# Optimization experiments

Measured on AMD Instinct MI355X. Metric: run time of the kernel, lower is better.

Reference implementation:

```python
import jax, jax.numpy as jnp
import numpy as np

T, B, IN, H, L = 512, 32, 512, 512, 2  # seq_len, batch, input_size, hidden_size, num_layers
D = 2  # bidirectional
EPS = 1e-5


def setup_inputs() -> dict:
    key = jax.random.key(0)
    ks = jax.random.split(key, 4)
    s = 0.05
    return {
        "x": jax.random.normal(ks[0], (T, B, IN), jnp.float32),
        "h0": jnp.zeros((L * D, B, H), jnp.float32),
        # stacked per (layer, direction) params; index = 2*layer + dir (dir 0 = fwd, 1 = back)
        "Wx": jax.random.normal(ks[1], (L * D, IN, 3 * H), jnp.float32) * s,
        "Wh": jax.random.normal(ks[2], (L * D, H, 3 * H), jnp.float32) * s,
        "bx": jnp.zeros((L * D, 3 * H), jnp.float32),
        "bh": jnp.zeros((L * D, 3 * H), jnp.float32),
        "gx": jnp.ones((L * D, 3 * H), jnp.float32),   # LN affine scale for input proj
        "bex": jnp.zeros((L * D, 3 * H), jnp.float32), # LN affine shift for input proj
        "gh": jnp.ones((L * D, 3 * H), jnp.float32),   # LN affine scale for recurrent proj
        "beh": jnp.zeros((L * D, 3 * H), jnp.float32), # LN affine shift for recurrent proj
    }


def _ln3(a, g, b):
    # per-gate LayerNorm: a is [B, 3H]; normalize each H-sized gate chunk
    Bn, H3 = a.shape
    Hh = H3 // 3
    a = a.reshape(Bn, 3, Hh)
    mu = a.mean(-1, keepdims=True)
    var = ((a - mu) ** 2).mean(-1, keepdims=True)
    a = (a - mu) * jax.lax.rsqrt(var + EPS)
    a = a * g.reshape(3, Hh) + b.reshape(3, Hh)
    return a.reshape(Bn, H3)


def _run_dir(xs, h, Wx, Wh, bx, bh, gx, bex, gh, beh):
    # xs: [T, B, F], h: [B, H]; scan LNGRU cell over time
    def step(h, x):
        ax = _ln3(x @ Wx + bx, gx, bex)
        ah = _ln3(h @ Wh + bh, gh, beh)
        axr, axz, axn = jnp.split(ax, 3, axis=-1)
        ahr, ahz, ahn = jnp.split(ah, 3, axis=-1)
        r = jax.nn.sigmoid(axr + ahr)
        z = jax.nn.sigmoid(axz + ahz)
        n = jnp.tanh(axn + r * ahn)
        h_new = (1.0 - z) * n + z * h
        return h_new, h_new
    hT, ys = jax.lax.scan(step, h, xs)
    return hT, ys


def reference(x, h0, Wx, Wh, bx, bh, gx, bex, gh, beh):
    ff, back = x, x
    hiddens = []
    for layer in range(L):
        i = 2 * layer
        hT, ff = _run_dir(ff, h0[i], Wx[i], Wh[i], bx[i], bh[i], gx[i], bex[i], gh[i], beh[i])
        hiddens.append(hT)
        j = 2 * layer + 1
        hT, yb = _run_dir(back[::-1], h0[j], Wx[j], Wh[j], bx[j], bh[j], gx[j], bex[j], gh[j], beh[j])
        back = yb[::-1]
        hiddens.append(hT)
    output = jnp.concatenate([ff, back], axis=-1)  # [T, B, 2H]
    return output, jnp.stack(hiddens)  # hiddens: [L*2, B, H]
```

## Files before the change

kernel.cpp:

```cpp
#include <hip/hip_runtime.h>

#define T_N 512
#define B_N 32
#define H_N 512
#define G3 1536
#define NBLK 192
#define NGRP 8
#define GRPSZ (NBLK / NGRP)
#define NT 1024
#define EPS_LN 1e-5f
#define OUT_HID_OFF (T_N * B_N * 1024)

#define WS_STATS 320
#define WS_DOTS  (WS_STATS + 1536)
#define WS_HBUF  (WS_DOTS + 4 * B_N * G3)
#define WS_Y0    (WS_HBUF + 2 * B_N * H_N)

#define WLDS_F 32256
#define HL_F   8256
#define LDS_BYTES ((WLDS_F + HL_F + 256) * 4)

__device__ __forceinline__ float cload(const float* p) {
  return __hip_atomic_load(p, __ATOMIC_RELAXED, __HIP_MEMORY_SCOPE_AGENT);
}
__device__ __forceinline__ void cstore(float* p, float v) {
  __hip_atomic_store(p, v, __ATOMIC_RELAXED, __HIP_MEMORY_SCOPE_AGENT);
}
union U64F2 { unsigned long long u; float f[2]; };
__device__ __forceinline__ U64F2 cload2(const float* p) {
  U64F2 r;
  r.u = __hip_atomic_load((const unsigned long long*)p, __ATOMIC_RELAXED,
                          __HIP_MEMORY_SCOPE_AGENT);
  return r;
}

__device__ __forceinline__ void gbar(unsigned* barbase, unsigned& epoch, int grp) {
  epoch++;
  __builtin_amdgcn_s_waitcnt(0);
  __syncthreads();
  if (threadIdx.x == 0) {
    unsigned* gc  = barbase + grp * 32;
    unsigned* top = barbase + NGRP * 32;
    unsigned* rel = barbase + NGRP * 32 + 32;
    unsigned r = __hip_atomic_fetch_add(gc, 1u, __ATOMIC_RELAXED, __HIP_MEMORY_SCOPE_AGENT);
    if (r == epoch * GRPSZ - 1u) {
      unsigned r2 = __hip_atomic_fetch_add(top, 1u, __ATOMIC_RELAXED, __HIP_MEMORY_SCOPE_AGENT);
      if (r2 == epoch * NGRP - 1u)
        __hip_atomic_store(rel, epoch, __ATOMIC_RELAXED, __HIP_MEMORY_SCOPE_AGENT);
    }
    while (__hip_atomic_load(rel, __ATOMIC_RELAXED, __HIP_MEMORY_SCOPE_AGENT) < epoch)
      __builtin_amdgcn_s_sleep(1);
  }
  __syncthreads();
}

#define FMA16(WA, WB, R1, R2) do { \
  acc[0][0][0]=fmaf((R1).x,(WA).x,acc[0][0][0]); acc[0][0][1]=fmaf((R1).y,(WA).y,acc[0][0][1]); \
  acc[0][0][2]=fmaf((R1).z,(WA).z,acc[0][0][2]); acc[0][0][3]=fmaf((R1).w,(WA).w,acc[0][0][3]); \
  acc[0][1][0]=fmaf((R2).x,(WA).x,acc[0][1][0]); acc[0][1][1]=fmaf((R2).y,(WA).y,acc[0][1][1]); \
  acc[0][1][2]=fmaf((R2).z,(WA).z,acc[0][1][2]); acc[0][1][3]=fmaf((R2).w,(WA).w,acc[0][1][3]); \
  acc[1][0][0]=fmaf((R1).x,(WB).x,acc[1][0][0]); acc[1][0][1]=fmaf((R1).y,(WB).y,acc[1][0][1]); \
  acc[1][0][2]=fmaf((R1).z,(WB).z,acc[1][0][2]); acc[1][0][3]=fmaf((R1).w,(WB).w,acc[1][0][3]); \
  acc[1][1][0]=fmaf((R2).x,(WB).x,acc[1][1][0]); acc[1][1][1]=fmaf((R2).y,(WB).y,acc[1][1][1]); \
  acc[1][1][2]=fmaf((R2).z,(WB).z,acc[1][1][2]); acc[1][1][3]=fmaf((R2).w,(WB).w,acc[1][1][3]); \
} while (0)

__global__ void __launch_bounds__(NT, 1)
lngru9(const float* __restrict__ x, const float* __restrict__ h0,
       const float* __restrict__ Wx, const float* __restrict__ Wh,
       const float* __restrict__ bx, const float* __restrict__ bh,
       const float* __restrict__ gx, const float* __restrict__ bex,
       const float* __restrict__ gh, const float* __restrict__ beh,
       float* __restrict__ out, float* __restrict__ ws)
{
  extern __shared__ __align__(16) float smem[];
  float* wlds = smem;
  float* hl   = smem + WLDS_F;
  float* sred = smem + WLDS_F + HL_F;

  unsigned* barbase = (unsigned*)ws;
  float* stats = ws + WS_STATS;
  float* dots  = ws + WS_DOTS;
  float* hbuf  = ws + WS_HBUF;
  float* y0    = ws + WS_Y0;

  const int tid  = threadIdx.x;
  const int lane = tid & 63;
  const int wv   = tid >> 6;
  const int bid  = blockIdx.x;
  const int grp  = bid & 7;
  const int bs   = bid & 1;
  const int jt   = (bid >> 1) % 24;
  const int kd   = (bid >> 1) / 24;
  const int kind = kd & 1;
  const int d    = kd >> 1;
  const int j0   = jt * 64;
  const int g    = jt >> 3;
  const int b0   = bs * 16;
  const bool is_gate = (kind == 0) && (jt < 8);

  const bool gw  = (wv < 4);
  const int jq   = wv & 3;
  const int jj   = lane & 7;
  const int boct = lane >> 3;
  const int jla  = jq * 8 + jj;
  const int jlb  = jla + 32;

  unsigned epoch = 0;

  for (int ph = 0; ph < 2; ++ph) {
    const int widx = ph * 2 + d;

    const float* wgl = (kind ? Wh : Wx) + (size_t)widx * H_N * G3 + j0;
    for (int kk = 0; kk < 32; ++kk) {
      int k = wv * 32 + kk;
      if (k < 504)
        wlds[(k >> 2) * 256 + lane * 4 + (k & 3)] = wgl[(size_t)k * G3 + lane];
    }
    float4 wt[2][2];
    if (gw) {
#pragma unroll
      for (int h = 0; h < 2; ++h) {
        wt[0][h].x = wgl[(size_t)(504 + 4*h + 0) * G3 + jla];
        wt[0][h].y = wgl[(size_t)(504 + 4*h + 1) * G3 + jla];
        wt[0][h].z = wgl[(size_t)(504 + 4*h + 2) * G3 + jla];
        wt[0][h].w = wgl[(size_t)(504 + 4*h + 3) * G3 + jla];
        wt[1][h].x = wgl[(size_t)(504 + 4*h + 0) * G3 + jlb];
        wt[1][h].y = wgl[(size_t)(504 + 4*h + 1) * G3 + jlb];
        wt[1][h].z = wgl[(size_t)(504 + 4*h + 2) * G3 + jlb];
        wt[1][h].w = wgl[(size_t)(504 + 4*h + 3) * G3 + jlb];
      }
    }

    if (is_gate) {
      cstore(&hbuf[(d * B_N + b0 + wv) * H_N + j0 + lane],
             h0[(widx * B_N + b0 + wv) * H_N + j0 + lane]);
    }
    gbar(barbase, epoch, grp);

    const float  bva  = (kind ? bh : bx)[widx * G3 + j0 + jla];
    const float  bvb  = (kind ? bh : bx)[widx * G3 + j0 + jlb];
    const float* xsrc = (ph == 0) ? x : (y0 + (size_t)d * T_N * B_N * H_N);
    const float* hsrc = hbuf + (d * B_N + b0) * H_N;
    const float4* wqa = (const float4*)wlds + jla;
    const float4* wqb = (const float4*)wlds + jlb;
    const float*  h1  = hl + boct * 516;
    const float*  h2  = hl + (boct + 8) * 516;

    for (int s = 0; s < T_N; ++s) {
      const int t = d ? (T_N - 1 - s) : s;
      const int p = s & 1;
      float* stp = stats + p * 768;

      if (kind) {
#pragma unroll
        for (int q = 0; q < 4; ++q) {
          int e = (tid + q * 1024) * 2;
          U64F2 v = cload2(hsrc + e);
          int bb = e >> 9, k = e & 511;
          hl[bb * 516 + k]     = v.f[0];
          hl[bb * 516 + k + 1] = v.f[1];
        }
        __syncthreads();
      }

      float acc[2][2][4] = {{{0.f,0.f,0.f,0.f},{0.f,0.f,0.f,0.f}},
                            {{0.f,0.f,0.f,0.f},{0.f,0.f,0.f,0.f}}};
      if (gw) {
        if (kind) {
#pragma unroll 3
          for (int k4 = 0; k4 < 126; ++k4) {
            float4 wa = wqa[k4 * 64];
            float4 wb = wqb[k4 * 64];
            float4 r1 = *(const float4*)(h1 + k4 * 4);
            float4 r2 = *(const float4*)(h2 + k4 * 4);
            FMA16(wa, wb, r1, r2);
          }
          {
            float4 r1a = *(const float4*)(h1 + 504);
            float4 r1b = *(const float4*)(h1 + 508);
            float4 r2a = *(const float4*)(h2 + 504);
            float4 r2b = *(const float4*)(h2 + 508);
            FMA16(wt[0][0], wt[1][0], r1a, r2a);
            FMA16(wt[0][1], wt[1][1], r1b, r2b);
          }
        } else {
          const float* rp1 = xsrc + ((size_t)t * B_N + b0 + boct) * H_N;
          const float* rp2 = rp1 + 8 * H_N;
#pragma unroll 6
          for (int k4 = 0; k4 < 126; ++k4) {
            float4 wa = wqa[k4 * 64];
            float4 wb = wqb[k4 * 64];
            float4 r1 = *(const float4*)(rp1 + k4 * 4);
            float4 r2 = *(const float4*)(rp2 + k4 * 4);
            FMA16(wa, wb, r1, r2);
          }
          {
            float4 r1a = *(const float4*)(rp1 + 504);
            float4 r1b = *(const float4*)(rp1 + 508);
            float4 r2a = *(const float4*)(rp2 + 504);
            float4 r2b = *(const float4*)(rp2 + 508);
            FMA16(wt[0][0], wt[1][0], r1a, r2a);
            FMA16(wt[0][1], wt[1][1], r1b, r2b);
          }
        }
      }

      if (gw) {
        float ta1 = bva + (acc[0][0][0] + acc[0][0][1]) + (acc[0][0][2] + acc[0][0][3]);
        float ta2 = bva + (acc[0][1][0] + acc[0][1][1]) + (acc[0][1][2] + acc[0][1][3]);
        float tb1 = bvb + (acc[1][0][0] + acc[1][0][1]) + (acc[1][0][2] + acc[1][0][3]);
        float tb2 = bvb + (acc[1][1][0] + acc[1][1][1]) + (acc[1][1][2] + acc[1][1][3]);

        float* dr1 = &dots[(size_t)(kd * B_N + b0 + boct) * G3 + j0];
        float* dr2 = dr1 + (size_t)8 * G3;
        cstore(dr1 + jla, ta1);
        cstore(dr1 + jlb, tb1);
        cstore(dr2 + jla, ta2);
        cstore(dr2 + jlb, tb2);

        float s1a = ta1 + tb1, s2a = ta1 * ta1 + tb1 * tb1;
        float s1b = ta2 + tb2, s2b = ta2 * ta2 + tb2 * tb2;
        s1a += __shfl_xor(s1a, 1, 64); s2a += __shfl_xor(s2a, 1, 64);
        s1b += __shfl_xor(s1b, 1, 64); s2b += __shfl_xor(s2b, 1, 64);
        s1a += __shfl_xor(s1a, 2, 64); s2a += __shfl_xor(s2a, 2, 64);
        s1b += __shfl_xor(s1b, 2, 64); s2b += __shfl_xor(s2b, 2, 64);
        s1a += __shfl_xor(s1a, 4, 64); s2a += __shfl_xor(s2a, 4, 64);
        s1b += __shfl_xor(s1b, 4, 64); s2b += __shfl_xor(s2b, 4, 64);
        if (jj == 0) {
          sred[(boct * 4 + jq) * 2 + 0] = s1a;
          sred[(boct * 4 + jq) * 2 + 1] = s2a;
          sred[((boct + 8) * 4 + jq) * 2 + 0] = s1b;
          sred[((boct + 8) * 4 + jq) * 2 + 1] = s2b;
        }
      }
      __syncthreads();
      if (tid < 32) {
        int bl = tid >> 1, st = tid & 1;
        float a2 = 0.f;
#pragma unroll
        for (int q = 0; q < 4; ++q) a2 += sred[(bl * 4 + q) * 2 + st];
        atomicAdd(&stp[((kd * 3 + g) * B_N + b0 + bl) * 2 + st], a2);
      }

      gbar(barbase, epoch, grp);

      if (bid == NBLK - 1) {
        float* so = stats + (p ^ 1) * 768;
        if (tid < 768) cstore(so + tid, 0.f);
      }
      if (is_gate) {
        const int c  = j0 + lane;
        const int gb = b0 + wv;
        float a[2][3];
#pragma unroll
        for (int k2 = 0; k2 < 2; ++k2) {
          const float* dr  = dots + ((d * 2 + k2) * B_N + gb) * G3;
          const float* gam = (k2 ? gh : gx) + widx * G3;
          const float* bet = (k2 ? beh : bex) + widx * G3;
#pragma unroll
          for (int g2 = 0; g2 < 3; ++g2) {
            float v = cload(dr + g2 * H_N + c);
            const float* sl = stp + (((d * 2 + k2) * 3 + g2) * B_N + gb) * 2;
            float mu  = cload(sl)     * (1.f / 512.f);
            float var = cload(sl + 1) * (1.f / 512.f) - mu * mu;
            float inv = rsqrtf(var + EPS_LN);
            int J = g2 * H_N + c;
            a[k2][g2] = (v - mu) * inv * gam[J] + bet[J];
          }
        }
        float r = 1.f / (1.f + __expf(-(a[0][0] + a[1][0])));
        float z = 1.f / (1.f + __expf(-(a[0][1] + a[1][1])));
        float n = tanhf(a[0][2] + r * a[1][2]);
        float* hp = hbuf + (d * B_N + gb) * H_N + c;
        float hnew = (1.f - z) * n + z * cload(hp);
        cstore(hp, hnew);
        if (ph == 0) {
          cstore(&y0[(((size_t)d * T_N + t) * B_N + gb) * H_N + c], hnew);
        } else {
          out[((size_t)t * B_N + gb) * 1024 + d * H_N + c] = hnew;
        }
        if (s == T_N - 1) {
          out[OUT_HID_OFF + (widx * B_N + gb) * H_N + c] = hnew;
        }
      }
      gbar(barbase, epoch, grp);
    }
  }
}

extern "C" void kernel_launch(void* const* d_in, const int* in_sizes, int n_in,
                              void* d_out, int out_size, void* d_ws, size_t ws_size,
                              hipStream_t stream) {
  const float* x    = (const float*)d_in[0];
  const float* h0   = (const float*)d_in[1];
  const float* Wx   = (const float*)d_in[2];
  const float* Wh   = (const float*)d_in[3];
  const float* bxp  = (const float*)d_in[4];
  const float* bhp  = (const float*)d_in[5];
  const float* gxp  = (const float*)d_in[6];
  const float* bexp = (const float*)d_in[7];
  const float* ghp  = (const float*)d_in[8];
  const float* behp = (const float*)d_in[9];
  float* out = (float*)d_out;
  float* ws  = (float*)d_ws;

  hipMemsetAsync(d_ws, 0, 8192, stream);

  hipFuncSetAttribute((const void*)lngru9,
                      hipFuncAttributeMaxDynamicSharedMemorySize, LDS_BYTES);

  void* args[] = {(void*)&x, (void*)&h0, (void*)&Wx, (void*)&Wh, (void*)&bxp, (void*)&bhp,
                  (void*)&gxp, (void*)&bexp, (void*)&ghp, (void*)&behp, (void*)&out, (void*)&ws};
  hipLaunchCooperativeKernel((void*)lngru9, dim3(NBLK), dim3(NT), args, LDS_BYTES, stream);
}
```

Measured before the change: 22.21 ms.

## Halve grid barriers per step by redundant gate update and pipelined input projection

Every recurrent-projection block now keeps its own copy of the batch's hidden state in LDS and recomputes the full gate update for 512 columns itself. This removes the global hbuf round-trip and one of the two grid barriers per timestep. The input projection is computed one step ahead into a triple-buffered slot, and the stats buffers are widened to four slots so zeroing can happen without an extra barrier. Each wave now handles four 8-column groups with two compute waves instead of four. The cost is redundant elementwise gate work in every kind=1 block, fewer active compute waves per block, and more workspace.

After: 27.09 ms. +22.0%, slower.

```diff
diff --git a/kernel.cpp b/kernel.cpp
--- a/kernel.cpp
+++ b/kernel.cpp
@@ -12,9 +12,11 @@
 #define OUT_HID_OFF (T_N * B_N * 1024)
 
 #define WS_STATS 320
-#define WS_DOTS  (WS_STATS + 1536)
-#define WS_HBUF  (WS_DOTS + 4 * B_N * G3)
-#define WS_Y0    (WS_HBUF + 2 * B_N * H_N)
+#define STSLOT   768
+#define WS_AXD   (WS_STATS + 4 * STSLOT)
+#define DSLOT    (2 * B_N * G3)
+#define WS_AHD   (WS_AXD + 3 * DSLOT)
+#define WS_Y0    (WS_AHD + 2 * DSLOT)
 
 #define WLDS_F 32256
 #define HL_F   8256
@@ -25,13 +27,6 @@
 }
 __device__ __forceinline__ void cstore(float* p, float v) {
   __hip_atomic_store(p, v, __ATOMIC_RELAXED, __HIP_MEMORY_SCOPE_AGENT);
-}
-union U64F2 { unsigned long long u; float f[2]; };
-__device__ __forceinline__ U64F2 cload2(const float* p) {
-  U64F2 r;
-  r.u = __hip_atomic_load((const unsigned long long*)p, __ATOMIC_RELAXED,
-                          __HIP_MEMORY_SCOPE_AGENT);
-  return r;
 }
 
 __device__ __forceinline__ void gbar(unsigned* barbase, unsigned& epoch, int grp) {
@@ -54,24 +49,20 @@
   __syncthreads();
 }
 
-#define FMA16(WA, WB, R1, R2) do { \
-  acc[0][0][0]=fmaf((R1).x,(WA).x,acc[0][0][0]); acc[0][0][1]=fmaf((R1).y,(WA).y,acc[0][0][1]); \
-  acc[0][0][2]=fmaf((R1).z,(WA).z,acc[0][0][2]); acc[0][0][3]=fmaf((R1).w,(WA).w,acc[0][0][3]); \
-  acc[0][1][0]=fmaf((R2).x,(WA).x,acc[0][1][0]); acc[0][1][1]=fmaf((R2).y,(WA).y,acc[0][1][1]); \
-  acc[0][1][2]=fmaf((R2).z,(WA).z,acc[0][1][2]); acc[0][1][3]=fmaf((R2).w,(WA).w,acc[0][1][3]); \
-  acc[1][0][0]=fmaf((R1).x,(WB).x,acc[1][0][0]); acc[1][0][1]=fmaf((R1).y,(WB).y,acc[1][0][1]); \
-  acc[1][0][2]=fmaf((R1).z,(WB).z,acc[1][0][2]); acc[1][0][3]=fmaf((R1).w,(WB).w,acc[1][0][3]); \
-  acc[1][1][0]=fmaf((R2).x,(WB).x,acc[1][1][0]); acc[1][1][1]=fmaf((R2).y,(WB).y,acc[1][1][1]); \
-  acc[1][1][2]=fmaf((R2).z,(WB).z,acc[1][1][2]); acc[1][1][3]=fmaf((R2).w,(WB).w,acc[1][1][3]); \
+#define FMA_M(M, W, R1, R2) do { \
+  acc[M][0][0]=fmaf((R1).x,(W).x,acc[M][0][0]); acc[M][0][1]=fmaf((R1).y,(W).y,acc[M][0][1]); \
+  acc[M][0][2]=fmaf((R1).z,(W).z,acc[M][0][2]); acc[M][0][3]=fmaf((R1).w,(W).w,acc[M][0][3]); \
+  acc[M][1][0]=fmaf((R2).x,(W).x,acc[M][1][0]); acc[M][1][1]=fmaf((R2).y,(W).y,acc[M][1][1]); \
+  acc[M][1][2]=fmaf((R2).z,(W).z,acc[M][1][2]); acc[M][1][3]=fmaf((R2).w,(W).w,acc[M][1][3]); \
 } while (0)
 
 __global__ void __launch_bounds__(NT, 1)
-lngru9(const float* __restrict__ x, const float* __restrict__ h0,
-       const float* __restrict__ Wx, const float* __restrict__ Wh,
-       const float* __restrict__ bx, const float* __restrict__ bh,
-       const float* __restrict__ gx, const float* __restrict__ bex,
-       const float* __restrict__ gh, const float* __restrict__ beh,
-       float* __restrict__ out, float* __restrict__ ws)
+lngru10(const float* __restrict__ x, const float* __restrict__ h0,
+        const float* __restrict__ Wx, const float* __restrict__ Wh,
+        const float* __restrict__ bx, const float* __restrict__ bh,
+        const float* __restrict__ gx, const float* __restrict__ bex,
+        const float* __restrict__ gh, const float* __restrict__ beh,
+        float* __restrict__ out, float* __restrict__ ws)
 {
   extern __shared__ __align__(16) float smem[];
   float* wlds = smem;
@@ -80,8 +71,8 @@
 
   unsigned* barbase = (unsigned*)ws;
   float* stats = ws + WS_STATS;
-  float* dots  = ws + WS_DOTS;
-  float* hbuf  = ws + WS_HBUF;
+  float* axd   = ws + WS_AXD;
+  float* ahd   = ws + WS_AHD;
   float* y0    = ws + WS_Y0;
 
   const int tid  = threadIdx.x;
@@ -97,19 +88,19 @@
   const int j0   = jt * 64;
   const int g    = jt >> 3;
   const int b0   = bs * 16;
-  const bool is_gate = (kind == 0) && (jt < 8);
-
-  const bool gw  = (wv < 4);
-  const int jq   = wv & 3;
+  const bool writer = (kind == 1) && (jt == 0);
+
+  const bool gw  = (wv < 2);
+  const int jq   = wv & 1;
   const int jj   = lane & 7;
   const int boct = lane >> 3;
-  const int jla  = jq * 8 + jj;
-  const int jlb  = jla + 32;
 
   unsigned epoch = 0;
 
   for (int ph = 0; ph < 2; ++ph) {
     const int widx = ph * 2 + d;
+
+    gbar(barbase, epoch, grp);
 
     const float* wgl = (kind ? Wh : Wx) + (size_t)widx * H_N * G3 + j0;
     for (int kk = 0; kk < 32; ++kk) {
@@ -117,110 +108,98 @@
       if (k < 504)
         wlds[(k >> 2) * 256 + lane * 4 + (k & 3)] = wgl[(size_t)k * G3 + lane];
     }
-    float4 wt[2][2];
+    float4 wt[4][2];
+    float  bva[4];
     if (gw) {
 #pragma unroll
-      for (int h = 0; h < 2; ++h) {
-        wt[0][h].x = wgl[(size_t)(504 + 4*h + 0) * G3 + jla];
-        wt[0][h].y = wgl[(size_t)(504 + 4*h + 1) * G3 + jla];
-        wt[0][h].z = wgl[(size_t)(504 + 4*h + 2) * G3 + jla];
-        wt[0][h].w = wgl[(size_t)(504 + 4*h + 3) * G3 + jla];
-        wt[1][h].x = wgl[(size_t)(504 + 4*h + 0) * G3 + jlb];
-        wt[1][h].y = wgl[(size_t)(504 + 4*h + 1) * G3 + jlb];
-        wt[1][h].z = wgl[(size_t)(504 + 4*h + 2) * G3 + jlb];
-        wt[1][h].w = wgl[(size_t)(504 + 4*h + 3) * G3 + jlb];
-      }
-    }
-
-    if (is_gate) {
-      cstore(&hbuf[(d * B_N + b0 + wv) * H_N + j0 + lane],
-             h0[(widx * B_N + b0 + wv) * H_N + j0 + lane]);
-    }
-    gbar(barbase, epoch, grp);
-
-    const float  bva  = (kind ? bh : bx)[widx * G3 + j0 + jla];
-    const float  bvb  = (kind ? bh : bx)[widx * G3 + j0 + jlb];
+      for (int m = 0; m < 4; ++m) {
+        const int jl = jq * 32 + m * 8 + jj;
+        bva[m] = (kind ? bh : bx)[widx * G3 + j0 + jl];
+#pragma unroll
+        for (int h = 0; h < 2; ++h) {
+          wt[m][h].x = wgl[(size_t)(504 + 4*h + 0) * G3 + jl];
+          wt[m][h].y = wgl[(size_t)(504 + 4*h + 1) * G3 + jl];
+          wt[m][h].z = wgl[(size_t)(504 + 4*h + 2) * G3 + jl];
+          wt[m][h].w = wgl[(size_t)(504 + 4*h + 3) * G3 + jl];
+        }
+      }
+    }
+    if (kind) {
+#pragma unroll
+      for (int q = 0; q < 8; ++q)
+        hl[wv * 516 + lane + 64*q] =
+            h0[((size_t)widx * B_N + b0 + wv) * H_N + lane + 64*q];
+    }
+    __syncthreads();
+
     const float* xsrc = (ph == 0) ? x : (y0 + (size_t)d * T_N * B_N * H_N);
-    const float* hsrc = hbuf + (d * B_N + b0) * H_N;
-    const float4* wqa = (const float4*)wlds + jla;
-    const float4* wqb = (const float4*)wlds + jlb;
-    const float*  h1  = hl + boct * 516;
-    const float*  h2  = hl + (boct + 8) * 516;
-
-    for (int s = 0; s < T_N; ++s) {
-      const int t = d ? (T_N - 1 - s) : s;
-      const int p = s & 1;
-      float* stp = stats + p * 768;
-
-      if (kind) {
-#pragma unroll
-        for (int q = 0; q < 4; ++q) {
-          int e = (tid + q * 1024) * 2;
-          U64F2 v = cload2(hsrc + e);
-          int bb = e >> 9, k = e & 511;
-          hl[bb * 516 + k]     = v.f[0];
-          hl[bb * 516 + k + 1] = v.f[1];
-        }
-        __syncthreads();
-      }
-
-      float acc[2][2][4] = {{{0.f,0.f,0.f,0.f},{0.f,0.f,0.f,0.f}},
-                            {{0.f,0.f,0.f,0.f},{0.f,0.f,0.f,0.f}}};
+    const float4* wbase = (const float4*)wlds + jq * 32 + jj;
+
+    auto run_step = [&](int ss) {
+      float acc[4][2][4] = {};
       if (gw) {
         if (kind) {
+          const float* h1 = hl + boct * 516;
+          const float* h2 = h1 + 8 * 516;
 #pragma unroll 3
           for (int k4 = 0; k4 < 126; ++k4) {
-            float4 wa = wqa[k4 * 64];
-            float4 wb = wqb[k4 * 64];
-            float4 r1 = *(const float4*)(h1 + k4 * 4);
-            float4 r2 = *(const float4*)(h2 + k4 * 4);
-            FMA16(wa, wb, r1, r2);
+            float4 w0 = wbase[k4*64 + 0];
+            float4 w1 = wbase[k4*64 + 8];
+            float4 w2 = wbase[k4*64 + 16];
+            float4 w3 = wbase[k4*64 + 24];
+            float4 r1 = *(const float4*)(h1 + k4*4);
+            float4 r2 = *(const float4*)(h2 + k4*4);
+            FMA_M(0,w0,r1,r2); FMA_M(1,w1,r1,r2);
+            FMA_M(2,w2,r1,r2); FMA_M(3,w3,r1,r2);
           }
-          {
-            float4 r1a = *(const float4*)(h1 + 504);
-            float4 r1b = *(const float4*)(h1 + 508);
-            float4 r2a = *(const float4*)(h2 + 504);
-            float4 r2b = *(const float4*)(h2 + 508);
-            FMA16(wt[0][0], wt[1][0], r1a, r2a);
-            FMA16(wt[0][1], wt[1][1], r1b, r2b);
-          }
+          float4 r1a = *(const float4*)(h1 + 504);
+          float4 r1b = *(const float4*)(h1 + 508);
+          float4 r2a = *(const float4*)(h2 + 504);
+          float4 r2b = *(const float4*)(h2 + 508);
+          FMA_M(0,wt[0][0],r1a,r2a); FMA_M(1,wt[1][0],r1a,r2a);
+          FMA_M(2,wt[2][0],r1a,r2a); FMA_M(3,wt[3][0],r1a,r2a);
+          FMA_M(0,wt[0][1],r1b,r2b); FMA_M(1,wt[1][1],r1b,r2b);
+          FMA_M(2,wt[2][1],r1b,r2b); FMA_M(3,wt[3][1],r1b,r2b);
         } else {
+          const int t = d ? (T_N - 1 - ss) : ss;
           const float* rp1 = xsrc + ((size_t)t * B_N + b0 + boct) * H_N;
           const float* rp2 = rp1 + 8 * H_N;
-#pragma unroll 6
+#pragma unroll 4
           for (int k4 = 0; k4 < 126; ++k4) {
-            float4 wa = wqa[k4 * 64];
-            float4 wb = wqb[k4 * 64];
-            float4 r1 = *(const float4*)(rp1 + k4 * 4);
-            float4 r2 = *(const float4*)(rp2 + k4 * 4);
-            FMA16(wa, wb, r1, r2);
+            float4 w0 = wbase[k4*64 + 0];
+            float4 w1 = wbase[k4*64 + 8];
+            float4 w2 = wbase[k4*64 + 16];
+            float4 w3 = wbase[k4*64 + 24];
+            float4 r1 = *(const float4*)(rp1 + k4*4);
+            float4 r2 = *(const float4*)(rp2 + k4*4);
+            FMA_M(0,w0,r1,r2); FMA_M(1,w1,r1,r2);
+            FMA_M(2,w2,r1,r2); FMA_M(3,w3,r1,r2);
           }
-          {
-            float4 r1a = *(const float4*)(rp1 + 504);
-            float4 r1b = *(const float4*)(rp1 + 508);
-            float4 r2a = *(const float4*)(rp2 + 504);
-            float4 r2b = *(const float4*)(rp2 + 508);
-            FMA16(wt[0][0], wt[1][0], r1a, r2a);
-            FMA16(wt[0][1], wt[1][1], r1b, r2b);
-          }
-        }
-      }
-
+          float4 r1a = *(const float4*)(rp1 + 504);
+          float4 r1b = *(const float4*)(rp1 + 508);
+          float4 r2a = *(const float4*)(rp2 + 504);
+          float4 r2b = *(const float4*)(rp2 + 508);
+          FMA_M(0,wt[0][0],r1a,r2a); FMA_M(1,wt[1][0],r1a,r2a);
+          FMA_M(2,wt[2][0],r1a,r2a); FMA_M(3,wt[3][0],r1a,r2a);
+          FMA_M(0,wt[0][1],r1b,r2b); FMA_M(1,wt[1][1],r1b,r2b);
+          FMA_M(2,wt[2][1],r1b,r2b); FMA_M(3,wt[3][1],r1b,r2b);
+        }
+      }
+      float* dd  = kind ? (ahd + (ss & 1) * DSLOT) : (axd + (ss % 3) * DSLOT);
+      float* stp = stats + (ss & 3) * STSLOT;
       if (gw) {
-        float ta1 = bva + (acc[0][0][0] + acc[0][0][1]) + (acc[0][0][2] + acc[0][0][3]);
-        float ta2 = bva + (acc[0][1][0] + acc[0][1][1]) + (acc[0][1][2] + acc[0][1][3]);
-        float tb1 = bvb + (acc[1][0][0] + acc[1][0][1]) + (acc[1][0][2] + acc[1][0][3]);
-        float tb2 = bvb + (acc[1][1][0] + acc[1][1][1]) + (acc[1][1][2] + acc[1][1][3]);
-
-        float* dr1 = &dots[(size_t)(kd * B_N + b0 + boct) * G3 + j0];
+        float* dr1 = dd + (size_t)(d * B_N + b0 + boct) * G3 + j0;
         float* dr2 = dr1 + (size_t)8 * G3;
-        cstore(dr1 + jla, ta1);
-        cstore(dr1 + jlb, tb1);
-        cstore(dr2 + jla, ta2);
-        cstore(dr2 + jlb, tb2);
-
-        float s1a = ta1 + tb1, s2a = ta1 * ta1 + tb1 * tb1;
-        float s1b = ta2 + tb2, s2b = ta2 * ta2 + tb2 * tb2;
+        float s1a = 0.f, s2a = 0.f, s1b = 0.f, s2b = 0.f;
+#pragma unroll
+        for (int m = 0; m < 4; ++m) {
+          const int jl = jq * 32 + m * 8 + jj;
+          float t1 = bva[m] + ((acc[m][0][0]+acc[m][0][1]) + (acc[m][0][2]+acc[m][0][3]));
+          float t2 = bva[m] + ((acc[m][1][0]+acc[m][1][1]) + (acc[m][1][2]+acc[m][1][3]));
+          cstore(dr1 + jl, t1);
+          cstore(dr2 + jl, t2);
+          s1a += t1; s2a += t1 * t1; s1b += t2; s2b += t2 * t2;
+        }
         s1a += __shfl_xor(s1a, 1, 64); s2a += __shfl_xor(s2a, 1, 64);
         s1b += __shfl_xor(s1b, 1, 64); s2b += __shfl_xor(s2b, 1, 64);
         s1a += __shfl_xor(s1a, 2, 64); s2a += __shfl_xor(s2a, 2, 64);
@@ -228,63 +207,87 @@
         s1a += __shfl_xor(s1a, 4, 64); s2a += __shfl_xor(s2a, 4, 64);
         s1b += __shfl_xor(s1b, 4, 64); s2b += __shfl_xor(s2b, 4, 64);
         if (jj == 0) {
-          sred[(boct * 4 + jq) * 2 + 0] = s1a;
-          sred[(boct * 4 + jq) * 2 + 1] = s2a;
-          sred[((boct + 8) * 4 + jq) * 2 + 0] = s1b;
-          sred[((boct + 8) * 4 + jq) * 2 + 1] = s2b;
+          sred[boct * 4 + jq * 2 + 0] = s1a;
+          sred[boct * 4 + jq * 2 + 1] = s2a;
+          sred[(boct + 8) * 4 + jq * 2 + 0] = s1b;
+          sred[(boct + 8) * 4 + jq * 2 + 1] = s2b;
         }
       }
       __syncthreads();
       if (tid < 32) {
         int bl = tid >> 1, st = tid & 1;
-        float a2 = 0.f;
-#pragma unroll
-        for (int q = 0; q < 4; ++q) a2 += sred[(bl * 4 + q) * 2 + st];
+        float a2 = sred[bl * 4 + st] + sred[bl * 4 + 2 + st];
         atomicAdd(&stp[((kd * 3 + g) * B_N + b0 + bl) * 2 + st], a2);
       }
+    };
+
+    if (!kind) run_step(0);
+    gbar(barbase, epoch, grp);
+
+    for (int s = 0; s < T_N; ++s) {
+      if (kind) run_step(s);
+      else if (s < T_N - 1) run_step(s + 1);
+
+      if (bid == NBLK - 1) {
+        float* so = stats + ((s + 2) & 3) * STSLOT;
+        if (tid < 768) cstore(so + tid, 0.f);
+      }
 
       gbar(barbase, epoch, grp);
 
-      if (bid == NBLK - 1) {
-        float* so = stats + (p ^ 1) * 768;
-        if (tid < 768) cstore(so + tid, 0.f);
-      }
-      if (is_gate) {
-        const int c  = j0 + lane;
+      if (kind) {
+        const int t  = d ? (T_N - 1 - s) : s;
         const int gb = b0 + wv;
-        float a[2][3];
-#pragma unroll
-        for (int k2 = 0; k2 < 2; ++k2) {
-          const float* dr  = dots + ((d * 2 + k2) * B_N + gb) * G3;
-          const float* gam = (k2 ? gh : gx) + widx * G3;
-          const float* bet = (k2 ? beh : bex) + widx * G3;
+        const float* axr = axd + (s % 3) * DSLOT + (size_t)(d * B_N + gb) * G3;
+        const float* ahr = ahd + (s & 1) * DSLOT + (size_t)(d * B_N + gb) * G3;
+        const float* stp = stats + (s & 3) * STSLOT;
+        float mu[2][3], inv[2][3];
+#pragma unroll
+        for (int k2 = 0; k2 < 2; ++k2)
 #pragma unroll
           for (int g2 = 0; g2 < 3; ++g2) {
-            float v = cload(dr + g2 * H_N + c);
             const float* sl = stp + (((d * 2 + k2) * 3 + g2) * B_N + gb) * 2;
-            float mu  = cload(sl)     * (1.f / 512.f);
-            float var = cload(sl + 1) * (1.f / 512.f) - mu * mu;
-            float inv = rsqrtf(var + EPS_LN);
-            int J = g2 * H_N + c;
-            a[k2][g2] = (v - mu) * inv * gam[J] + bet[J];
+            float m1 = cload(sl)     * (1.f / 512.f);
+            float m2 = cload(sl + 1) * (1.f / 512.f);
+            mu[k2][g2]  = m1;
+            inv[k2][g2] = rsqrtf(m2 - m1 * m1 + EPS_LN);
           }
-        }
-        float r = 1.f / (1.f + __expf(-(a[0][0] + a[1][0])));
-        float z = 1.f / (1.f + __expf(-(a[0][1] + a[1][1])));
-        float n = tanhf(a[0][2] + r * a[1][2]);
-        float* hp = hbuf + (d * B_N + gb) * H_N + c;
-        float hnew = (1.f - z) * n + z * cload(hp);
-        cstore(hp, hnew);
-        if (ph == 0) {
-          cstore(&y0[(((size_t)d * T_N + t) * B_N + gb) * H_N + c], hnew);
-        } else {
-          out[((size_t)t * B_N + gb) * 1024 + d * H_N + c] = hnew;
-        }
-        if (s == T_N - 1) {
-          out[OUT_HID_OFF + (widx * B_N + gb) * H_N + c] = hnew;
-        }
-      }
-      gbar(barbase, epoch, grp);
+        const float* gxr = gx  + widx * G3;
+        const float* bxr = bex + widx * G3;
+        const float* ghr = gh  + widx * G3;
+        const float* bhr = beh + widx * G3;
+#pragma unroll 2
+        for (int q = 0; q < 8; ++q) {
+          const int c = lane + 64 * q;
+          float ax0 = cload(axr + c);
+          float ax1 = cload(axr + H_N + c);
+          float ax2 = cload(axr + 2 * H_N + c);
+          float ah0 = cload(ahr + c);
+          float ah1 = cload(ahr + H_N + c);
+          float ah2 = cload(ahr + 2 * H_N + c);
+          float a00 = (ax0 - mu[0][0]) * inv[0][0] * gxr[c]           + bxr[c];
+          float a01 = (ax1 - mu[0][1]) * inv[0][1] * gxr[H_N + c]     + bxr[H_N + c];
+          float a02 = (ax2 - mu[0][2]) * inv[0][2] * gxr[2*H_N + c]   + bxr[2*H_N + c];
+          float a10 = (ah0 - mu[1][0]) * inv[1][0] * ghr[c]           + bhr[c];
+          float a11 = (ah1 - mu[1][1]) * inv[1][1] * ghr[H_N + c]     + bhr[H_N + c];
+          float a12 = (ah2 - mu[1][2]) * inv[1][2] * ghr[2*H_N + c]   + bhr[2*H_N + c];
+          float r = 1.f / (1.f + __expf(-(a00 + a10)));
+          float z = 1.f / (1.f + __expf(-(a01 + a11)));
+          float n = tanhf(a02 + r * a12);
+          float* hp = hl + wv * 516 + c;
+          float hnew = (1.f - z) * n + z * *hp;
+          *hp = hnew;
+          if (writer) {
+            if (ph == 0)
+              cstore(&y0[(((size_t)d * T_N + t) * B_N + gb) * H_N + c], hnew);
+            else
+              out[((size_t)t * B_N + gb) * 1024 + d * H_N + c] = hnew;
+            if (s == T_N - 1)
+              out[OUT_HID_OFF + ((size_t)widx * B_N + gb) * H_N + c] = hnew;
+          }
+        }
+        __syncthreads();
+      }
     }
   }
 }
@@ -305,12 +308,12 @@
   float* out = (float*)d_out;
   float* ws  = (float*)d_ws;
 
-  hipMemsetAsync(d_ws, 0, 8192, stream);
-
-  hipFuncSetAttribute((const void*)lngru9,
+  hipMemsetAsync(d_ws, 0, 16384, stream);
+
+  hipFuncSetAttribute((const void*)lngru10,
                       hipFuncAttributeMaxDynamicSharedMemorySize, LDS_BYTES);
 
   void* args[] = {(void*)&x, (void*)&h0, (void*)&Wx, (void*)&Wh, (void*)&bxp, (void*)&bhp,
                   (void*)&gxp, (void*)&bexp, (void*)&ghp, (void*)&behp, (void*)&out, (void*)&ws};
-  hipLaunchCooperativeKernel((void*)lngru9, dim3(NBLK), dim3(NT), args, LDS_BYTES, stream);
-}
+  hipLaunchCooperativeKernel((void*)lngru10, dim3(NBLK), dim3(NT), args, LDS_BYTES, stream);
+}
```
